# Performance work log

Measured on AMD Instinct MI355X. Metric: run time of the kernel, lower is better.

Reference implementation:

```python
import jax, jax.numpy as jnp
import numpy as np

N_HEAD = 8
D_MODEL = 1024   # also the sequence length L (the code requires L == d_model)
D_K = 256
D_V = 256
D_TRANS = 256
B = 32
KS = 13
PAD = 6
LN_EPS = 1e-3
TEMPER = float(np.sqrt(D_MODEL))


def conv1d(x, w, b):
    # x: (B, Cin, L), w: (Cout, Cin, K) torch layout, 'same' padding 6
    y = jax.lax.conv_general_dilated(
        x, w, window_strides=(1,), padding=[(PAD, PAD)],
        dimension_numbers=('NCH', 'OIH', 'NCH'))
    return y + b[None, :, None]


def setup_inputs() -> dict:
    key = jax.random.key(0)
    ks = jax.random.split(key, 16)
    n = lambda i, shape, s=1.0: jax.random.normal(ks[i], shape, jnp.float32) * s
    return {
        'q': n(0, (B, D_K, D_MODEL)),
        'k': n(1, (B, D_K, D_MODEL)),
        'v': n(2, (B, D_V, D_MODEL)),
        'cq_w': n(3, (D_TRANS, D_K, KS), 0.02), 'cq_b': jnp.zeros((D_TRANS,), jnp.float32),
        'ck_w': n(4, (D_TRANS, D_K, KS), 0.02), 'ck_b': jnp.zeros((D_TRANS,), jnp.float32),
        'cv_w': n(5, (D_TRANS, D_V, KS), 0.02), 'cv_b': jnp.zeros((D_TRANS,), jnp.float32),
        'w_qs': n(6, (N_HEAD, D_MODEL, D_TRANS), 0.02),
        'w_ks': n(7, (N_HEAD, D_MODEL, D_TRANS), 0.02),
        'w_vs': n(8, (N_HEAD, D_MODEL, D_TRANS), 0.02),
        'proj_w': n(9, (D_MODEL, N_HEAD * D_TRANS), 0.02),
        'proj_b': jnp.zeros((D_MODEL,), jnp.float32),
        'fc_w': n(10, (D_V, D_TRANS, KS), 0.02), 'fc_b': jnp.zeros((D_V,), jnp.float32),
        'ln_a': jnp.ones((D_MODEL,), jnp.float32),
        'ln_b': jnp.zeros((D_MODEL,), jnp.float32),
    }


def reference(q, k, v, cq_w, cq_b, ck_w, ck_b, cv_w, cv_b,
              w_qs, w_ks, w_vs, proj_w, proj_b, fc_w, fc_b, ln_a, ln_b):
    # Conv1d QKV "projections": (B, d_k, L) -> (B, d_trans, L)
    q_b = conv1d(q, cq_w, cq_b)
    k_b = conv1d(k, ck_w, ck_b)
    v_b = conv1d(v, cv_w, cv_b)

    # Per-head projection along the L (==d_model) axis:
    # torch: (H, B*d_trans, L) bmm (H, L, d_trans) -> (H*B, d_trans, d_trans)
    q_s = jnp.einsum('btl,hld->hbtd', q_b, w_qs)  # (H, B, Dt, Dt)
    k_s = jnp.einsum('btl,hld->hbtd', k_b, w_ks)
    v_s = jnp.einsum('btl,hld->hbtd', v_b, w_vs)

    # Scaled dot-product attention over the d_trans axis (eval mode: dropout off)
    scores = jnp.einsum('hbqd,hbkd->hbqk', q_s, k_s) / TEMPER
    attn = jax.nn.softmax(scores, axis=-1)
    out = jnp.einsum('hbqk,hbkd->hbqd', attn, v_s)  # (H, B, Dt, Dt)

    # torch: split heads along batch dim, concat along last -> (B, Dt, H*Dt)
    outputs = out.transpose(1, 2, 0, 3).reshape(B, D_TRANS, N_HEAD * D_TRANS)
    outputs = outputs @ proj_w.T + proj_b            # (B, Dt, d_model)
    outputs = conv1d(outputs, fc_w, fc_b)            # (B, d_v, d_model)

    # Custom LayerNorm over last axis with unbiased std and eps added to sigma
    z = outputs + q
    mu = jnp.mean(z, axis=-1, keepdims=True)
    sigma = jnp.std(z, axis=-1, ddof=1, keepdims=True)
    output = (z - mu) / (sigma + LN_EPS) * ln_a + ln_b

    attns = attn.reshape(N_HEAD * B, D_TRANS, D_TRANS)
    return output, attns
```

## Files before the change

### kernel.cpp

```cpp
#include <hip/hip_runtime.h>

typedef unsigned short u16;
typedef __attribute__((ext_vector_type(8))) short short8;
typedef __attribute__((ext_vector_type(4))) float f32x4;

__device__ __forceinline__ float bf2f(u16 x) {
  unsigned u = ((unsigned)x) << 16;
  return __builtin_bit_cast(float, u);
}
__device__ __forceinline__ u16 f2bf(float x) {
  unsigned u = __builtin_bit_cast(unsigned, x);
  u += 0x7fffu + ((u >> 16) & 1u);
  return (u16)(u >> 16);
}

__device__ __forceinline__ void gl2lds16(const u16* g, u16* l) {
  __builtin_amdgcn_global_load_lds(
      (const __attribute__((address_space(1))) unsigned*)g,
      (__attribute__((address_space(3))) unsigned*)l, 16, 0, 0);
}

__global__ void detect_kernel(const void* ln_a, unsigned* flag) {
  if (threadIdx.x == 0 && blockIdx.x == 0)
    *flag = (*(const unsigned*)ln_a == 0x3F800000u) ? 1u : 0u;
}

#define GEMM_TILE(T, DO_STAGE, VMCNT, ENDBAR)                                 \
  {                                                                           \
    const u16* ring_ = smem + ((T) & 3) * 12288;                              \
    short8 af_[4], bq_[4];                                                    \
    _Pragma("unroll") for (int i_ = 0; i_ < 4; i_++)                          \
        af_[i_] = *(const short8*)(ring_ + offA[i_]);                         \
    _Pragma("unroll") for (int j_ = 0; j_ < 4; j_++)                          \
        bq_[j_] = *(const short8*)(ring_ + offB[j_]);                         \
    if (DO_STAGE) stage_tile((T) + 3);                                        \
    __builtin_amdgcn_s_barrier();                                             \
    asm volatile("s_waitcnt lgkmcnt(0)" ::: "memory");                        \
    __builtin_amdgcn_sched_barrier(0);                                        \
    __builtin_amdgcn_s_setprio(1);                                            \
    _Pragma("unroll") for (int i_ = 0; i_ < 4; i_++)                          \
        _Pragma("unroll") for (int j_ = 0; j_ < 4; j_++)                      \
            acc[i_][j_] = __builtin_amdgcn_mfma_f32_16x16x32_bf16(            \
                af_[i_], bq_[j_], acc[i_][j_], 0, 0, 0);                      \
    __builtin_amdgcn_s_setprio(0);                                            \
    if ((VMCNT) == 6) asm volatile("s_waitcnt vmcnt(6)" ::: "memory");        \
    else if ((VMCNT) == 3) asm volatile("s_waitcnt vmcnt(3)" ::: "memory");   \
    else if ((VMCNT) == 0) asm volatile("s_waitcnt vmcnt(0)" ::: "memory");   \
    if (ENDBAR) __builtin_amdgcn_s_barrier();                                 \
  }

template <typename OutT>
__global__ __launch_bounds__(512, 2) void gemm_kernel(
    const u16* __restrict__ A, const u16* __restrict__ B, OutT* __restrict__ C,
    const u16* __restrict__ bias, int K, int lda, int ldb, int ldc,
    long a0, long a1, long a2, long b0, long b1, long b2,
    long c0, long c1, long c2, int biasMid, float alpha) {
  extern __shared__ u16 smem[];

  const int tid = threadIdx.x;
  const int z = blockIdx.z;
  const int zlo = z & 31, zmid = (z >> 5) & 7, zhi = z >> 8;
  const u16* Ab = A + (long)zlo * a0 + (long)zmid * a1 + (long)zhi * a2;
  const u16* Bb = B + (long)zlo * b0 + (long)zmid * b1 + (long)zhi * b2;
  OutT* Cb = C + (long)zlo * c0 + (long)zmid * c1 + (long)zhi * c2;
  const int m0 = blockIdx.y * 256;
  const int n0 = blockIdx.x * 128;

  const int wave = tid >> 6;
  const int lane = tid & 63;

  const int lgrp = lane >> 3;
  const int slot = lane & 7;
  const u16* gsrc[3];
  int ldsoff[3];
#pragma unroll
  for (int c = 0; c < 3; c++) {
    const int L0 = (c < 2 ? c * 64 : 0) + wave * 8;
    const int L = L0 + lgrp;
    const int ls = slot ^ (L & 7);
    const int row = 2 * L + (ls >> 2);
    const int blk = ls & 3;
    if (c < 2) {
      gsrc[c] = Ab + (long)(m0 + row) * lda + blk * 8;
      ldsoff[c] = L0 * 64;
    } else {
      gsrc[c] = Bb + (long)(n0 + row) * ldb + blk * 8;
      ldsoff[c] = 8192 + L0 * 64;
    }
  }

  auto stage_tile = [&](int t) {
    u16* dst = smem + (t & 3) * 12288;
    const long koff = (long)t * 32;
#pragma unroll
    for (int c = 0; c < 3; c++) gl2lds16(gsrc[c] + koff, dst + ldsoff[c]);
  };

  const int wm = (wave >> 1) * 64;
  const int wn = (wave & 1) * 64;
  const int quad = lane >> 4;
  const int r = lane & 15;
  int offA[4], offB[4];
#pragma unroll
  for (int i = 0; i < 4; i++) {
    const int rowA = wm + i * 16 + r;
    const int lnA = rowA >> 1;
    offA[i] = lnA * 64 + ((((rowA & 1) * 4 + quad) ^ (lnA & 7)) * 8);
    const int rowB = wn + i * 16 + r;
    const int lnB = rowB >> 1;
    offB[i] = 8192 + lnB * 64 + ((((rowB & 1) * 4 + quad) ^ (lnB & 7)) * 8);
  }

  f32x4 acc[4][4] = {};
  const int nt = K >> 5;

  stage_tile(0);
  stage_tile(1);
  stage_tile(2);
  asm volatile("s_waitcnt vmcnt(6)" ::: "memory");
  __builtin_amdgcn_s_barrier();

  int t = 0;
  for (; t < nt - 3; ++t) GEMM_TILE(t, true, 6, true);
  GEMM_TILE(t, false, 3, true);
  ++t;
  GEMM_TILE(t, false, 0, true);
  ++t;
  GEMM_TILE(t, false, -1, false);

  const u16* biasb = bias ? bias + (long)zmid * biasMid : nullptr;
#pragma unroll
  for (int i = 0; i < 4; i++) {
#pragma unroll
    for (int rr = 0; rr < 4; rr++) {
      const int mg = m0 + wm + i * 16 + quad * 4 + rr;
      const float bv = biasb ? bf2f(biasb[mg]) : 0.0f;
#pragma unroll
      for (int j = 0; j < 4; j++) {
        const int ng = n0 + wn + j * 16 + r;
        float val = acc[i][j][rr] * alpha + bv;
        if constexpr (__is_same(OutT, float))
          Cb[(long)mg * ldc + ng] = val;
        else
          Cb[(long)mg * ldc + ng] = f2bf(val);
      }
    }
  }
}

__global__ __launch_bounds__(256) void transpose_kernel(
    const void* __restrict__ i0, const void* __restrict__ i1,
    const void* __restrict__ i2, u16* __restrict__ out, int R, int C,
    long ostride, int ooff, int zdiv, const unsigned* __restrict__ flagp) {
  const bool f32 = *flagp != 0;
  __shared__ u16 t[64 * 68];
  const int z = blockIdx.z;
  const void* in = (z < zdiv) ? i0 : (z < 2 * zdiv) ? i1 : i2;
  const int zq = (z < zdiv) ? z : (z < 2 * zdiv) ? z - zdiv : z - 2 * zdiv;
  const long ibase = (long)zq * R * C;
  const int r0 = blockIdx.y * 64;
  const int c0 = blockIdx.x * 64;
  u16* ob = out + (long)z * ostride + ooff;
  const int tid = threadIdx.x;
#pragma unroll
  for (int i = 0; i < 4; i++) {
    const int vv = tid + i * 256;
    const int rr = vv >> 4;
    const int cc = (vv & 15) << 2;
    uint2 packed;
    if (f32) {
      const float4 fv = *(const float4*)((const float*)in + ibase +
                                         (long)(r0 + rr) * C + (c0 + cc));
      packed.x = (unsigned)f2bf(fv.x) | ((unsigned)f2bf(fv.y) << 16);
      packed.y = (unsigned)f2bf(fv.z) | ((unsigned)f2bf(fv.w) << 16);
    } else {
      packed = *(const uint2*)((const u16*)in + ibase + (long)(r0 + rr) * C +
                               (c0 + cc));
    }
    *(uint2*)(&t[rr * 68 + cc]) = packed;
  }
  __syncthreads();
#pragma unroll
  for (int i = 0; i < 4; i++) {
    const int vv = tid + i * 256;
    const int cc = vv >> 4;
    const int rr = (vv & 15) << 2;
    unsigned lo = (unsigned)t[rr * 68 + cc] | ((unsigned)t[(rr + 1) * 68 + cc] << 16);
    unsigned hi =
        (unsigned)t[(rr + 2) * 68 + cc] | ((unsigned)t[(rr + 3) * 68 + cc] << 16);
    uint2 val = {lo, hi};
    *(uint2*)(ob + (long)(c0 + cc) * R + (r0 + rr)) = val;
  }
}

__global__ __launch_bounds__(256) void pack_w_kernel(
    const void* __restrict__ w0, const void* __restrict__ w1,
    const void* __restrict__ w2, const void* __restrict__ w3,
    u16* __restrict__ out, const unsigned* __restrict__ flagp) {
  const bool f32 = *flagp != 0;
  const int y = blockIdx.y;
  const void* in = (y == 0) ? w0 : (y == 1) ? w1 : (y == 2) ? w2 : w3;
  u16* o = out + (long)y * 851968;
  const int t = blockIdx.x * 256 + threadIdx.x;
  const int co = t / 3328;
  const int rem = t - co * 3328;
  const int dk = rem >> 8;
  const int ci = rem & 255;
  const int src = co * 3328 + ci * 13 + dk;
  o[t] = f32 ? f2bf(((const float*)in)[src]) : ((const u16*)in)[src];
}

__global__ __launch_bounds__(256) void cvt_kernel(const void* __restrict__ in,
                                                  u16* __restrict__ out, long n,
                                                  const unsigned* __restrict__ flagp) {
  const bool f32 = *flagp != 0;
  const long i = ((long)blockIdx.x * 256 + threadIdx.x) * 8;
  if (i >= n) return;
  if (f32) {
    const float* p = (const float*)in + i;
    const float4 a = *(const float4*)p;
    const float4 b = *(const float4*)(p + 4);
    uint4 o;
    o.x = (unsigned)f2bf(a.x) | ((unsigned)f2bf(a.y) << 16);
    o.y = (unsigned)f2bf(a.z) | ((unsigned)f2bf(a.w) << 16);
    o.z = (unsigned)f2bf(b.x) | ((unsigned)f2bf(b.y) << 16);
    o.w = (unsigned)f2bf(b.z) | ((unsigned)f2bf(b.w) << 16);
    *(uint4*)(out + i) = o;
  } else {
    *(uint4*)(out + i) = *(const uint4*)((const u16*)in + i);
  }
}

__global__ __launch_bounds__(256) void bias_cvt_kernel(
    const void* __restrict__ s0, const void* __restrict__ s1,
    const void* __restrict__ s2, const void* __restrict__ s3,
    const void* __restrict__ s4, u16* __restrict__ out,
    const unsigned* __restrict__ flagp) {
  const bool f32 = *flagp != 0;
  const long i = threadIdx.x * 8;
  const void* src;
  long off;
  if (i < 256) { src = s0; off = i; }
  else if (i < 512) { src = s1; off = i - 256; }
  else if (i < 768) { src = s2; off = i - 512; }
  else if (i < 1024) { src = s3; off = i - 768; }
  else { src = s4; off = i - 1024; }
  if (f32) {
    const float* p = (const float*)src + off;
    const float4 a = *(const float4*)p;
    const float4 b = *(const float4*)(p + 4);
    uint4 o;
    o.x = (unsigned)f2bf(a.x) | ((unsigned)f2bf(a.y) << 16);
    o.y = (unsigned)f2bf(a.z) | ((unsigned)f2bf(a.w) << 16);
    o.z = (unsigned)f2bf(b.x) | ((unsigned)f2bf(b.y) << 16);
    o.w = (unsigned)f2bf(b.z) | ((unsigned)f2bf(b.w) << 16);
    *(uint4*)(out + i) = o;
  } else {
    *(uint4*)(out + i) = *(const uint4*)((const u16*)src + off);
  }
}

__global__ __launch_bounds__(256) void zeropad_kernel(u16* __restrict__ base,
                                                      long bstride, int nb) {
  const int t = blockIdx.x * 256 + threadIdx.x;
  if (t >= nb * 384) return;
  const int b = t / 384;
  const int rem = t - b * 384;
  const int rp = rem >> 5;
  const int col = (rem & 31) * 8;
  const int row = rp < 6 ? rp : 1024 + rp;
  uint4 zz = {0u, 0u, 0u, 0u};
  *(uint4*)(base + (long)b * bstride + row * 256 + col) = zz;
}

__global__ __launch_bounds__(256) void softmax_kernel(
    u16* __restrict__ sc, void* __restrict__ dout,
    const unsigned* __restrict__ flagp) {
  const bool f32 = *flagp != 0;
  const long row = (long)blockIdx.x * 4 + (threadIdx.x >> 6);
  const int lane = threadIdx.x & 63;
  const uint2 raw = *(const uint2*)(sc + row * 256 + lane * 4);
  float s0 = bf2f((u16)(raw.x & 0xffff)), s1 = bf2f((u16)(raw.x >> 16));
  float s2 = bf2f((u16)(raw.y & 0xffff)), s3 = bf2f((u16)(raw.y >> 16));
  float m = fmaxf(fmaxf(s0, s1), fmaxf(s2, s3));
  for (int o = 32; o > 0; o >>= 1) m = fmaxf(m, __shfl_xor(m, o, 64));
  float e0 = expf(s0 - m), e1 = expf(s1 - m), e2 = expf(s2 - m), e3 = expf(s3 - m);
  float sum = e0 + e1 + e2 + e3;
  for (int o = 32; o > 0; o >>= 1) sum += __shfl_xor(sum, o, 64);
  const float inv = 1.0f / sum;
  const float p0 = e0 * inv, p1 = e1 * inv, p2 = e2 * inv, p3 = e3 * inv;
  uint2 ov;
  ov.x = (unsigned)f2bf(p0) | ((unsigned)f2bf(p1) << 16);
  ov.y = (unsigned)f2bf(p2) | ((unsigned)f2bf(p3) << 16);
  *(uint2*)(sc + row * 256 + lane * 4) = ov;
  if (f32) {
    float4 o4 = {p0, p1, p2, p3};
    *(float4*)((float*)dout + 8388608 + row * 256 + lane * 4) = o4;
  } else {
    *(uint2*)((u16*)dout + 8388608 + row * 256 + lane * 4) = ov;
  }
}

__global__ __launch_bounds__(256) void ln_kernel(
    const float* __restrict__ fc, const void* __restrict__ qraw,
    const void* __restrict__ la, const void* __restrict__ lb,
    void* __restrict__ dout, const unsigned* __restrict__ flagp) {
  const bool f32 = *flagp != 0;
  __shared__ float red[4];
  const long row = blockIdx.x;
  const int tid = threadIdx.x;
  const int col = tid * 4;
  const float4 zf = *(const float4*)(fc + row * 1024 + col);
  float q0, q1, q2, q3;
  if (f32) {
    const float4 t = *(const float4*)((const float*)qraw + row * 1024 + col);
    q0 = t.x; q1 = t.y; q2 = t.z; q3 = t.w;
  } else {
    const uint2 qr = *(const uint2*)((const u16*)qraw + row * 1024 + col);
    q0 = bf2f((u16)(qr.x & 0xffff)); q1 = bf2f((u16)(qr.x >> 16));
    q2 = bf2f((u16)(qr.y & 0xffff)); q3 = bf2f((u16)(qr.y >> 16));
  }
  const float z0 = zf.x + q0, z1 = zf.y + q1, z2 = zf.z + q2, z3 = zf.w + q3;
  float s = z0 + z1 + z2 + z3;
  for (int o = 32; o > 0; o >>= 1) s += __shfl_xor(s, o, 64);
  if ((tid & 63) == 0) red[tid >> 6] = s;
  __syncthreads();
  const float mu = (red[0] + red[1] + red[2] + red[3]) * (1.0f / 1024.0f);
  __syncthreads();
  const float d0 = z0 - mu, d1 = z1 - mu, d2 = z2 - mu, d3 = z3 - mu;
  float ss = d0 * d0 + d1 * d1 + d2 * d2 + d3 * d3;
  for (int o = 32; o > 0; o >>= 1) ss += __shfl_xor(ss, o, 64);
  if ((tid & 63) == 0) red[tid >> 6] = ss;
  __syncthreads();
  const float var = (red[0] + red[1] + red[2] + red[3]) * (1.0f / 1023.0f);
  const float inv = 1.0f / (sqrtf(var) + 1e-3f);
  float a0, a1, a2, a3, b0, b1, b2, b3;
  if (f32) {
    const float4 ta = *(const float4*)((const float*)la + col);
    const float4 tb = *(const float4*)((const float*)lb + col);
    a0 = ta.x; a1 = ta.y; a2 = ta.z; a3 = ta.w;
    b0 = tb.x; b1 = tb.y; b2 = tb.z; b3 = tb.w;
  } else {
    const uint2 ta = *(const uint2*)((const u16*)la + col);
    const uint2 tb = *(const uint2*)((const u16*)lb + col);
    a0 = bf2f((u16)(ta.x & 0xffff)); a1 = bf2f((u16)(ta.x >> 16));
    a2 = bf2f((u16)(ta.y & 0xffff)); a3 = bf2f((u16)(ta.y >> 16));
    b0 = bf2f((u16)(tb.x & 0xffff)); b1 = bf2f((u16)(tb.x >> 16));
    b2 = bf2f((u16)(tb.y & 0xffff)); b3 = bf2f((u16)(tb.y >> 16));
  }
  const float o0 = d0 * inv * a0 + b0, o1 = d1 * inv * a1 + b1;
  const float o2v = d2 * inv * a2 + b2, o3 = d3 * inv * a3 + b3;
  if (f32) {
    float4 o4 = {o0, o1, o2v, o3};
    *(float4*)((float*)dout + row * 1024 + col) = o4;
  } else {
    uint2 o2;
    o2.x = (unsigned)f2bf(o0) | ((unsigned)f2bf(o1) << 16);
    o2.y = (unsigned)f2bf(o2v) | ((unsigned)f2bf(o3) << 16);
    *(uint2*)((u16*)dout + row * 1024 + col) = o2;
  }
}

enum : long {
  OWPQ = 0,
  OWPK = 851968,
  OWPV = 1703936,
  OWPFC = 2555904,
  OWQT = 3407872,
  OWKT = 5505024,
  OWVT = 7602176,
  OPW16 = 9699328,
  OBQKV = 11796480,
  OBFC = 11797248,
  OBPROJ = 11797504,
  OFLAG = 11798528,
  OQB = 11798536,
  OKB = 20187144,
  OVB = 28575752,
  OQS = 36964360,
  OKS = 53741576,
  OVST = 70518792,
  OXPAD = OQS,
  OSC = OQB,
  OOUTC = OQS,
  OPROJP = OKS,
  OFC = OVST,
};

extern "C" void kernel_launch(void* const* d_in, const int* in_sizes, int n_in,
                              void* d_out, int out_size, void* d_ws,
                              size_t ws_size, hipStream_t stream) {
  const void* q = d_in[0];
  const void* k = d_in[1];
  const void* v = d_in[2];
  const void* cq_w = d_in[3];
  const void* cq_b = d_in[4];
  const void* ck_w = d_in[5];
  const void* ck_b = d_in[6];
  const void* cv_w = d_in[7];
  const void* cv_b = d_in[8];
  const void* w_qs = d_in[9];
  const void* w_ks = d_in[10];
  const void* w_vs = d_in[11];
  const void* proj_w = d_in[12];
  const void* proj_b = d_in[13];
  const void* fc_w = d_in[14];
  const void* fc_b = d_in[15];
  const void* ln_a = d_in[16];
  const void* ln_b = d_in[17];

  u16* ws = (u16*)d_ws;
  unsigned* flag = (unsigned*)(ws + OFLAG);

  static int attr_done = 0;
  if (!attr_done) {
    hipFuncSetAttribute(reinterpret_cast<const void*>(&gemm_kernel<u16>),
                        hipFuncAttributeMaxDynamicSharedMemorySize, 98304);
    hipFuncSetAttribute(reinterpret_cast<const void*>(&gemm_kernel<float>),
                        hipFuncAttributeMaxDynamicSharedMemorySize, 98304);
    attr_done = 1;
  }

  detect_kernel<<<1, 64, 0, stream>>>(ln_a, flag);

  pack_w_kernel<<<dim3(3328, 4), 256, 0, stream>>>(cq_w, ck_w, cv_w, fc_w,
                                                   ws + OWPQ, flag);
  transpose_kernel<<<dim3(4, 16, 24), 256, 0, stream>>>(
      w_qs, w_ks, w_vs, ws + OWQT, 1024, 256, 262144, 0, 8, flag);
  cvt_kernel<<<1024, 256, 0, stream>>>(proj_w, ws + OPW16, 2097152, flag);
  bias_cvt_kernel<<<1, 256, 0, stream>>>(cq_b, ck_b, cv_b, fc_b, proj_b,
                                         ws + OBQKV, flag);

  zeropad_kernel<<<144, 256, 0, stream>>>(ws + OXPAD, 265216, 96);
  transpose_kernel<<<dim3(16, 4, 96), 256, 0, stream>>>(
      q, k, v, ws + OXPAD, 256, 1024, 265216, 1536, 32, flag);

  gemm_kernel<u16><<<dim3(8, 1, 96), 512, 98304, stream>>>(
      ws + OWPQ, ws + OXPAD, ws + OQB, ws + OBQKV, 3328, 3328, 256, 1024,
      0, 851968, 0, 265216, 8486912, 0, 262144, 8388608, 0, 256, 1.0f);

  gemm_kernel<u16><<<dim3(2, 1, 512), 512, 98304, stream>>>(
      ws + OQB, ws + OWQT, ws + OQS, nullptr, 1024, 1024, 1024, 256,
      262144, 0, 8388608, 0, 262144, 2097152, 65536, 2097152, 16777216, 0, 1.0f);
  gemm_kernel<u16><<<dim3(2, 1, 256), 512, 98304, stream>>>(
      ws + OWVT, ws + OVB, ws + OVST, nullptr, 1024, 1024, 1024, 256,
      0, 262144, 0, 262144, 0, 0, 65536, 2097152, 0, 0, 1.0f);

  gemm_kernel<u16><<<dim3(2, 1, 256), 512, 98304, stream>>>(
      ws + OQS, ws + OKS, ws + OSC, nullptr, 256, 256, 256, 256,
      65536, 2097152, 0, 65536, 2097152, 0, 65536, 2097152, 0, 0, 0.03125f);

  softmax_kernel<<<16384, 256, 0, stream>>>(ws + OSC, d_out, flag);

  gemm_kernel<u16><<<dim3(2, 1, 256), 512, 98304, stream>>>(
      ws + OSC, ws + OVST, ws + OOUTC, nullptr, 256, 256, 256, 2048,
      65536, 2097152, 0, 65536, 2097152, 0, 524288, 256, 0, 0, 1.0f);

  zeropad_kernel<<<48, 256, 0, stream>>>(ws + OPROJP, 265216, 32);
  gemm_kernel<u16><<<dim3(2, 4, 32), 512, 98304, stream>>>(
      ws + OPW16, ws + OOUTC, ws + OPROJP + 1536, ws + OBPROJ, 2048, 2048, 2048,
      256, 0, 0, 0, 524288, 0, 0, 265216, 0, 0, 0, 1.0f);

  gemm_kernel<float><<<dim3(8, 1, 32), 512, 98304, stream>>>(
      ws + OWPFC, ws + OPROJP, (float*)(ws + OFC), ws + OBFC, 3328, 3328, 256,
      1024, 0, 0, 0, 265216, 0, 0, 262144, 0, 0, 0, 1.0f);

  ln_kernel<<<8192, 256, 0, stream>>>((const float*)(ws + OFC), q, ln_a, ln_b,
                                      d_out, flag);

  (void)in_sizes; (void)n_in; (void)out_size; (void)ws_size;
}
```

Before: 815.8 us.

## Add wide 256x256 GEMM tile variant with 3-stage ring for batched GEMMs

Adds a WIDE template variant of the GEMM kernel that computes a 256x256 output tile per block, with each of the 8 waves owning a 128x64 sub-tile. This halves the number of B-operand reloads per output element. The LDS buffer grows to 16384 elements and the prefetch ring shrinks from 4 stages to 3 to fit the same 96KB. The conv-QKV, per-head projection, scores and attn*V GEMMs switch to it with half the grid. The trade-off is a doubled accumulator footprint (128 floats per lane), which risks register pressure against launch_bounds(512,2), plus a shallower prefetch pipeline and fewer blocks in flight.

```diff
diff --git a/kernel.cpp b/kernel.cpp
--- a/kernel.cpp
+++ b/kernel.cpp
@@ -25,15 +25,15 @@
     *flag = (*(const unsigned*)ln_a == 0x3F800000u) ? 1u : 0u;
 }
 
-#define GEMM_TILE(T, DO_STAGE, VMCNT, ENDBAR)                                 \
+#define GEMM_TILE(T, RB, DO_STAGE, SB, VMCNT, ENDBAR)                         \
   {                                                                           \
-    const u16* ring_ = smem + ((T) & 3) * 12288;                              \
+    const u16* ring_ = smem + (RB)*BUF;                                       \
     short8 af_[4], bq_[4];                                                    \
     _Pragma("unroll") for (int i_ = 0; i_ < 4; i_++)                          \
         af_[i_] = *(const short8*)(ring_ + offA[i_]);                         \
     _Pragma("unroll") for (int j_ = 0; j_ < 4; j_++)                          \
         bq_[j_] = *(const short8*)(ring_ + offB[j_]);                         \
-    if (DO_STAGE) stage_tile((T) + 3);                                        \
+    if (DO_STAGE) stage_tile((T) + AHEAD, (SB));                              \
     __builtin_amdgcn_s_barrier();                                             \
     asm volatile("s_waitcnt lgkmcnt(0)" ::: "memory");                        \
     __builtin_amdgcn_sched_barrier(0);                                        \
@@ -43,19 +43,38 @@
             acc[i_][j_] = __builtin_amdgcn_mfma_f32_16x16x32_bf16(            \
                 af_[i_], bq_[j_], acc[i_][j_], 0, 0, 0);                      \
     __builtin_amdgcn_s_setprio(0);                                            \
+    if constexpr (WIDE) {                                                     \
+      _Pragma("unroll") for (int i_ = 0; i_ < 4; i_++)                        \
+          af_[i_] = *(const short8*)(ring_ + offA[4 + i_]);                   \
+      asm volatile("s_waitcnt lgkmcnt(0)" ::: "memory");                      \
+      __builtin_amdgcn_sched_barrier(0);                                      \
+      __builtin_amdgcn_s_setprio(1);                                          \
+      _Pragma("unroll") for (int i_ = 0; i_ < 4; i_++)                        \
+          _Pragma("unroll") for (int j_ = 0; j_ < 4; j_++)                    \
+              acc[4 + i_][j_] = __builtin_amdgcn_mfma_f32_16x16x32_bf16(      \
+                  af_[i_], bq_[j_], acc[4 + i_][j_], 0, 0, 0);                \
+      __builtin_amdgcn_s_setprio(0);                                          \
+    }                                                                         \
     if ((VMCNT) == 6) asm volatile("s_waitcnt vmcnt(6)" ::: "memory");        \
+    else if ((VMCNT) == 4) asm volatile("s_waitcnt vmcnt(4)" ::: "memory");   \
     else if ((VMCNT) == 3) asm volatile("s_waitcnt vmcnt(3)" ::: "memory");   \
     else if ((VMCNT) == 0) asm volatile("s_waitcnt vmcnt(0)" ::: "memory");   \
     if (ENDBAR) __builtin_amdgcn_s_barrier();                                 \
   }
 
-template <typename OutT>
+template <typename OutT, bool WIDE>
 __global__ __launch_bounds__(512, 2) void gemm_kernel(
     const u16* __restrict__ A, const u16* __restrict__ B, OutT* __restrict__ C,
     const u16* __restrict__ bias, int K, int lda, int ldb, int ldc,
     long a0, long a1, long a2, long b0, long b1, long b2,
     long c0, long c1, long c2, int biasMid, float alpha) {
   extern __shared__ u16 smem[];
+  constexpr int BN = WIDE ? 256 : 128;
+  constexpr int BUF = WIDE ? 16384 : 12288;
+  constexpr int RING = WIDE ? 3 : 4;
+  constexpr int AHEAD = RING - 1;
+  constexpr int NCALL = WIDE ? 4 : 3;
+  constexpr int MI = WIDE ? 8 : 4;
 
   const int tid = threadIdx.x;
   const int z = blockIdx.z;
@@ -64,23 +83,24 @@
   const u16* Bb = B + (long)zlo * b0 + (long)zmid * b1 + (long)zhi * b2;
   OutT* Cb = C + (long)zlo * c0 + (long)zmid * c1 + (long)zhi * c2;
   const int m0 = blockIdx.y * 256;
-  const int n0 = blockIdx.x * 128;
+  const int n0 = blockIdx.x * BN;
 
   const int wave = tid >> 6;
   const int lane = tid & 63;
 
   const int lgrp = lane >> 3;
   const int slot = lane & 7;
-  const u16* gsrc[3];
-  int ldsoff[3];
-#pragma unroll
-  for (int c = 0; c < 3; c++) {
-    const int L0 = (c < 2 ? c * 64 : 0) + wave * 8;
+  const u16* gsrc[NCALL];
+  int ldsoff[NCALL];
+#pragma unroll
+  for (int c = 0; c < NCALL; c++) {
+    const bool isA = (c < 2);
+    const int L0 = (isA ? c : (c - 2)) * 64 + wave * 8;
     const int L = L0 + lgrp;
     const int ls = slot ^ (L & 7);
     const int row = 2 * L + (ls >> 2);
     const int blk = ls & 3;
-    if (c < 2) {
+    if (isA) {
       gsrc[c] = Ab + (long)(m0 + row) * lda + blk * 8;
       ldsoff[c] = L0 * 64;
     } else {
@@ -89,48 +109,61 @@
     }
   }
 
-  auto stage_tile = [&](int t) {
-    u16* dst = smem + (t & 3) * 12288;
+  auto stage_tile = [&](int t, int buf) {
+    u16* dst = smem + buf * BUF;
     const long koff = (long)t * 32;
 #pragma unroll
-    for (int c = 0; c < 3; c++) gl2lds16(gsrc[c] + koff, dst + ldsoff[c]);
+    for (int c = 0; c < NCALL; c++) gl2lds16(gsrc[c] + koff, dst + ldsoff[c]);
   };
 
-  const int wm = (wave >> 1) * 64;
-  const int wn = (wave & 1) * 64;
+  const int wm = WIDE ? ((wave >> 2) * 128) : ((wave >> 1) * 64);
+  const int wn = WIDE ? ((wave & 3) * 64) : ((wave & 1) * 64);
   const int quad = lane >> 4;
   const int r = lane & 15;
-  int offA[4], offB[4];
-#pragma unroll
-  for (int i = 0; i < 4; i++) {
+  int offA[MI], offB[4];
+#pragma unroll
+  for (int i = 0; i < MI; i++) {
     const int rowA = wm + i * 16 + r;
     const int lnA = rowA >> 1;
     offA[i] = lnA * 64 + ((((rowA & 1) * 4 + quad) ^ (lnA & 7)) * 8);
-    const int rowB = wn + i * 16 + r;
+  }
+#pragma unroll
+  for (int j = 0; j < 4; j++) {
+    const int rowB = wn + j * 16 + r;
     const int lnB = rowB >> 1;
-    offB[i] = 8192 + lnB * 64 + ((((rowB & 1) * 4 + quad) ^ (lnB & 7)) * 8);
-  }
-
-  f32x4 acc[4][4] = {};
+    offB[j] = 8192 + lnB * 64 + ((((rowB & 1) * 4 + quad) ^ (lnB & 7)) * 8);
+  }
+
+  f32x4 acc[MI][4] = {};
   const int nt = K >> 5;
 
-  stage_tile(0);
-  stage_tile(1);
-  stage_tile(2);
-  asm volatile("s_waitcnt vmcnt(6)" ::: "memory");
+#pragma unroll
+  for (int i = 0; i < AHEAD; i++) stage_tile(i, i);
+  if constexpr (WIDE)
+    asm volatile("s_waitcnt vmcnt(4)" ::: "memory");
+  else
+    asm volatile("s_waitcnt vmcnt(6)" ::: "memory");
   __builtin_amdgcn_s_barrier();
 
-  int t = 0;
-  for (; t < nt - 3; ++t) GEMM_TILE(t, true, 6, true);
-  GEMM_TILE(t, false, 3, true);
+  int t = 0, rbuf = 0, sbuf = AHEAD;
+  for (; t < nt - AHEAD; ++t) {
+    GEMM_TILE(t, rbuf, true, sbuf, (WIDE ? 4 : 6), true);
+    rbuf = (rbuf + 1 == RING) ? 0 : rbuf + 1;
+    sbuf = (sbuf + 1 == RING) ? 0 : sbuf + 1;
+  }
+  if constexpr (!WIDE) {
+    GEMM_TILE(t, rbuf, false, 0, 3, true);
+    ++t;
+    rbuf = (rbuf + 1 == RING) ? 0 : rbuf + 1;
+  }
+  GEMM_TILE(t, rbuf, false, 0, 0, true);
   ++t;
-  GEMM_TILE(t, false, 0, true);
-  ++t;
-  GEMM_TILE(t, false, -1, false);
+  rbuf = (rbuf + 1 == RING) ? 0 : rbuf + 1;
+  GEMM_TILE(t, rbuf, false, 0, -1, false);
 
   const u16* biasb = bias ? bias + (long)zmid * biasMid : nullptr;
 #pragma unroll
-  for (int i = 0; i < 4; i++) {
+  for (int i = 0; i < MI; i++) {
 #pragma unroll
     for (int rr = 0; rr < 4; rr++) {
       const int mg = m0 + wm + i * 16 + quad * 4 + rr;
@@ -414,9 +447,11 @@
 
   static int attr_done = 0;
   if (!attr_done) {
-    hipFuncSetAttribute(reinterpret_cast<const void*>(&gemm_kernel<u16>),
+    hipFuncSetAttribute(reinterpret_cast<const void*>(&gemm_kernel<u16, true>),
                         hipFuncAttributeMaxDynamicSharedMemorySize, 98304);
-    hipFuncSetAttribute(reinterpret_cast<const void*>(&gemm_kernel<float>),
+    hipFuncSetAttribute(reinterpret_cast<const void*>(&gemm_kernel<u16, false>),
+                        hipFuncAttributeMaxDynamicSharedMemorySize, 98304);
+    hipFuncSetAttribute(reinterpret_cast<const void*>(&gemm_kernel<float, false>),
                         hipFuncAttributeMaxDynamicSharedMemorySize, 98304);
     attr_done = 1;
   }
@@ -435,33 +470,33 @@
   transpose_kernel<<<dim3(16, 4, 96), 256, 0, stream>>>(
       q, k, v, ws + OXPAD, 256, 1024, 265216, 1536, 32, flag);
 
-  gemm_kernel<u16><<<dim3(8, 1, 96), 512, 98304, stream>>>(
+  gemm_kernel<u16, true><<<dim3(4, 1, 96), 512, 98304, stream>>>(
       ws + OWPQ, ws + OXPAD, ws + OQB, ws + OBQKV, 3328, 3328, 256, 1024,
       0, 851968, 0, 265216, 8486912, 0, 262144, 8388608, 0, 256, 1.0f);
 
-  gemm_kernel<u16><<<dim3(2, 1, 512), 512, 98304, stream>>>(
+  gemm_kernel<u16, true><<<dim3(1, 1, 512), 512, 98304, stream>>>(
       ws + OQB, ws + OWQT, ws + OQS, nullptr, 1024, 1024, 1024, 256,
       262144, 0, 8388608, 0, 262144, 2097152, 65536, 2097152, 16777216, 0, 1.0f);
-  gemm_kernel<u16><<<dim3(2, 1, 256), 512, 98304, stream>>>(
+  gemm_kernel<u16, true><<<dim3(1, 1, 256), 512, 98304, stream>>>(
       ws + OWVT, ws + OVB, ws + OVST, nullptr, 1024, 1024, 1024, 256,
       0, 262144, 0, 262144, 0, 0, 65536, 2097152, 0, 0, 1.0f);
 
-  gemm_kernel<u16><<<dim3(2, 1, 256), 512, 98304, stream>>>(
+  gemm_kernel<u16, true><<<dim3(1, 1, 256), 512, 98304, stream>>>(
       ws + OQS, ws + OKS, ws + OSC, nullptr, 256, 256, 256, 256,
       65536, 2097152, 0, 65536, 2097152, 0, 65536, 2097152, 0, 0, 0.03125f);
 
   softmax_kernel<<<16384, 256, 0, stream>>>(ws + OSC, d_out, flag);
 
-  gemm_kernel<u16><<<dim3(2, 1, 256), 512, 98304, stream>>>(
+  gemm_kernel<u16, true><<<dim3(1, 1, 256), 512, 98304, stream>>>(
       ws + OSC, ws + OVST, ws + OOUTC, nullptr, 256, 256, 256, 2048,
       65536, 2097152, 0, 65536, 2097152, 0, 524288, 256, 0, 0, 1.0f);
 
   zeropad_kernel<<<48, 256, 0, stream>>>(ws + OPROJP, 265216, 32);
-  gemm_kernel<u16><<<dim3(2, 4, 32), 512, 98304, stream>>>(
+  gemm_kernel<u16, false><<<dim3(2, 4, 32), 512, 98304, stream>>>(
       ws + OPW16, ws + OOUTC, ws + OPROJP + 1536, ws + OBPROJ, 2048, 2048, 2048,
       256, 0, 0, 0, 524288, 0, 0, 265216, 0, 0, 0, 1.0f);
 
-  gemm_kernel<float><<<dim3(8, 1, 32), 512, 98304, stream>>>(
+  gemm_kernel<float, false><<<dim3(8, 1, 32), 512, 98304, stream>>>(
       ws + OWPFC, ws + OPROJP, (float*)(ws + OFC), ws + OBFC, 3328, 3328, 256,
       1024, 0, 0, 0, 265216, 0, 0, 262144, 0, 0, 0, 1.0f);
 
```

Result: faster. 794.2 us (-2.6%).
